# Performance work log

Hardware: AMD Instinct MI355X
Metric: run time of the kernel (lower is better)

## Reference

```python
import jax, jax.numpy as jnp
import numpy as np
from jax import lax

# Four fixed 3x3 directional difference kernels, stacked as OIHW [4,1,3,3]
_KL = np.array([[0, 0, 0], [-1, 1, 0], [0, 0, 0]], dtype=np.float32)
_KR = np.array([[0, 0, 0], [0, 1, -1], [0, 0, 0]], dtype=np.float32)
_KU = np.array([[0, -1, 0], [0, 1, 0], [0, 0, 0]], dtype=np.float32)
_KD = np.array([[0, 0, 0], [0, 1, 0], [0, -1, 0]], dtype=np.float32)
DIR_KERNELS = jnp.asarray(np.stack([_KL, _KR, _KU, _KD])[:, None, :, :])  # [4,1,3,3]


def _avg_pool4(x):
    # x: [B,1,H,W] with H,W divisible by 4 -> [B,1,H/4,W/4]
    B, C, H, W = x.shape
    return x.reshape(B, C, H // 4, 4, W // 4, 4).mean(axis=(3, 5))


def _dir_diffs(x):
    # x: [B,1,h,w] -> [B,4,h,w], 3x3 conv with zero padding 1 (SAME)
    return lax.conv_general_dilated(
        x, DIR_KERNELS,
        window_strides=(1, 1), padding=((1, 1), (1, 1)),
        dimension_numbers=('NCHW', 'OIHW', 'NCHW'))


def setup_inputs() -> dict:
    key = jax.random.key(0)
    k1, k2 = jax.random.split(key)
    org = jax.random.uniform(k1, (32, 3, 512, 512), dtype=jnp.float32)
    enhance = jax.random.uniform(k2, (32, 3, 512, 512), dtype=jnp.float32)
    return {"org": org, "enhance": enhance}


def reference(org, enhance):
    org_pool = _avg_pool4(org.mean(axis=1, keepdims=True))          # [B,1,h,w]
    enh_pool = _avg_pool4(enhance.mean(axis=1, keepdims=True))      # [B,1,h,w]
    d = _dir_diffs(org_pool) - _dir_diffs(enh_pool)                  # [B,4,h,w]
    E = jnp.sum(d * d, axis=1, keepdims=True)                        # [B,1,h,w]
    return E
```

## Files before the change

kernel.cpp:

```cpp
#include <hip/hip_runtime.h>


typedef float f4 __attribute__((ext_vector_type(4)));

__global__ __launch_bounds__(256) void pool_diff_kernel(
    const f4* __restrict__ org, const f4* __restrict__ enh,
    float* __restrict__ p) {
  __shared__ float red[128];
  int t = threadIdx.x;
  int s = blockIdx.x;
  int b = s >> 7;
  int py = s & 127;
  int sb = b * 196608 + py * 512;

  int j0 = sb + t;
  f4 A0 = __builtin_nontemporal_load(&org[j0]);
  f4 B0 = __builtin_nontemporal_load(&enh[j0]);
  f4 A1 = __builtin_nontemporal_load(&org[j0 + 65536]);
  f4 B1 = __builtin_nontemporal_load(&enh[j0 + 65536]);
  f4 A2 = __builtin_nontemporal_load(&org[j0 + 131072]);
  f4 B2 = __builtin_nontemporal_load(&enh[j0 + 131072]);
  f4 acc = (A0 - B0) + (A1 - B1) + (A2 - B2);

  int j1 = j0 + 256;
  f4 C0 = __builtin_nontemporal_load(&org[j1]);
  f4 D0 = __builtin_nontemporal_load(&enh[j1]);
  f4 C1 = __builtin_nontemporal_load(&org[j1 + 65536]);
  f4 D1 = __builtin_nontemporal_load(&enh[j1 + 65536]);
  f4 C2 = __builtin_nontemporal_load(&org[j1 + 131072]);
  f4 D2 = __builtin_nontemporal_load(&enh[j1 + 131072]);
  acc += (C0 - D0) + (C1 - D1) + (C2 - D2);

  float mine = acc.x + acc.y + acc.z + acc.w;
  if (t >= 128) red[t - 128] = mine;
  __syncthreads();
  if (t < 128) {
    p[b * 16384 + py * 128 + t] = (mine + red[t]) * (1.0f / 48.0f);
  }
}

__global__ __launch_bounds__(256) void espa_stencil_kernel(
    const float* __restrict__ p, float* __restrict__ out) {
  int idx = blockIdx.x * 256 + threadIdx.x;
  int x = idx & 127;
  int y = (idx >> 7) & 127;
  float c = p[idx];
  float l = (x > 0)   ? p[idx - 1]   : 0.f;
  float r = (x < 127) ? p[idx + 1]   : 0.f;
  float u = (y > 0)   ? p[idx - 128] : 0.f;
  float d = (y < 127) ? p[idx + 128] : 0.f;
  float dl = c - l, dr = c - r, du = c - u, dd = c - d;
  out[idx] = dl * dl + dr * dr + du * du + dd * dd;
}

extern "C" void kernel_launch(void* const* d_in, const int* in_sizes, int n_in,
                              void* d_out, int out_size, void* d_ws, size_t ws_size,
                              hipStream_t stream) {
  const f4* org = (const f4*)d_in[0];
  const f4* enh = (const f4*)d_in[1];
  float* p   = (float*)d_ws;
  float* out = (float*)d_out;

  pool_diff_kernel<<<4096, 256, 0, stream>>>(org, enh, p);
  const int N = 32 * 128 * 128;
  espa_stencil_kernel<<<N / 256, 256, 0, stream>>>(p, out);
}
```

Measured before the change: 197.4 us.

## Pool per channel with 16 loads in flight, sum channels in stencil

The pooling kernel now gives each block one channel of one image and four pooled rows. Each thread issues 16 independent vector loads instead of 12, which raises memory-level parallelism. The three per-channel pooled maps go to workspace, and the stencil kernel sums and scales them at each neighbor access. This trades a larger intermediate and about 15 scattered reads per output in the stencil for deeper load concurrency in the bandwidth-bound pass.

```diff
diff --git a/kernel.cpp b/kernel.cpp
--- a/kernel.cpp
+++ b/kernel.cpp
@@ -3,52 +3,77 @@
 
 typedef float f4 __attribute__((ext_vector_type(4)));
 
-__global__ __launch_bounds__(256) void pool_diff_kernel(
+__global__ __launch_bounds__(256) void pool_channel_kernel(
     const f4* __restrict__ org, const f4* __restrict__ enh,
-    float* __restrict__ p) {
-  __shared__ float red[128];
+    float* __restrict__ pc) {
+  __shared__ float red[4][128];
   int t = threadIdx.x;
   int s = blockIdx.x;
-  int b = s >> 7;
-  int py = s & 127;
-  int sb = b * 196608 + py * 512;
+  int g  = s & 31;
+  int bc = s >> 5;
+  int base = bc * 65536 + g * 2048;
 
-  int j0 = sb + t;
-  f4 A0 = __builtin_nontemporal_load(&org[j0]);
-  f4 B0 = __builtin_nontemporal_load(&enh[j0]);
-  f4 A1 = __builtin_nontemporal_load(&org[j0 + 65536]);
-  f4 B1 = __builtin_nontemporal_load(&enh[j0 + 65536]);
-  f4 A2 = __builtin_nontemporal_load(&org[j0 + 131072]);
-  f4 B2 = __builtin_nontemporal_load(&enh[j0 + 131072]);
-  f4 acc = (A0 - B0) + (A1 - B1) + (A2 - B2);
+  int h  = t >> 7;
+  int px = t & 127;
 
-  int j1 = j0 + 256;
-  f4 C0 = __builtin_nontemporal_load(&org[j1]);
-  f4 D0 = __builtin_nontemporal_load(&enh[j1]);
-  f4 C1 = __builtin_nontemporal_load(&org[j1 + 65536]);
-  f4 D1 = __builtin_nontemporal_load(&enh[j1 + 65536]);
-  f4 C2 = __builtin_nontemporal_load(&org[j1 + 131072]);
-  f4 D2 = __builtin_nontemporal_load(&enh[j1 + 131072]);
-  acc += (C0 - D0) + (C1 - D1) + (C2 - D2);
+  int j = base + t;
+  f4 o0 = __builtin_nontemporal_load(&org[j +    0]);
+  f4 o1 = __builtin_nontemporal_load(&org[j +  256]);
+  f4 o2 = __builtin_nontemporal_load(&org[j +  512]);
+  f4 o3 = __builtin_nontemporal_load(&org[j +  768]);
+  f4 o4 = __builtin_nontemporal_load(&org[j + 1024]);
+  f4 o5 = __builtin_nontemporal_load(&org[j + 1280]);
+  f4 o6 = __builtin_nontemporal_load(&org[j + 1536]);
+  f4 o7 = __builtin_nontemporal_load(&org[j + 1792]);
+  f4 e0 = __builtin_nontemporal_load(&enh[j +    0]);
+  f4 e1 = __builtin_nontemporal_load(&enh[j +  256]);
+  f4 e2 = __builtin_nontemporal_load(&enh[j +  512]);
+  f4 e3 = __builtin_nontemporal_load(&enh[j +  768]);
+  f4 e4 = __builtin_nontemporal_load(&enh[j + 1024]);
+  f4 e5 = __builtin_nontemporal_load(&enh[j + 1280]);
+  f4 e6 = __builtin_nontemporal_load(&enh[j + 1536]);
+  f4 e7 = __builtin_nontemporal_load(&enh[j + 1792]);
 
-  float mine = acc.x + acc.y + acc.z + acc.w;
-  if (t >= 128) red[t - 128] = mine;
+  f4 d0 = (o0 - e0) + (o1 - e1);
+  f4 d1 = (o2 - e2) + (o3 - e3);
+  f4 d2 = (o4 - e4) + (o5 - e5);
+  f4 d3 = (o6 - e6) + (o7 - e7);
+  float a0 = d0.x + d0.y + d0.z + d0.w;
+  float a1 = d1.x + d1.y + d1.z + d1.w;
+  float a2 = d2.x + d2.y + d2.z + d2.w;
+  float a3 = d3.x + d3.y + d3.z + d3.w;
+
+  if (h == 1) {
+    red[0][px] = a0; red[1][px] = a1; red[2][px] = a2; red[3][px] = a3;
+  }
   __syncthreads();
-  if (t < 128) {
-    p[b * 16384 + py * 128 + t] = (mine + red[t]) * (1.0f / 48.0f);
+  if (h == 0) {
+    int ob = bc * 16384 + g * 4 * 128 + px;
+    pc[ob +   0] = a0 + red[0][px];
+    pc[ob + 128] = a1 + red[1][px];
+    pc[ob + 256] = a2 + red[2][px];
+    pc[ob + 384] = a3 + red[3][px];
   }
 }
 
-__global__ __launch_bounds__(256) void espa_stencil_kernel(
-    const float* __restrict__ p, float* __restrict__ out) {
+__global__ __launch_bounds__(256) void combine_stencil_kernel(
+    const float* __restrict__ pc, float* __restrict__ out) {
   int idx = blockIdx.x * 256 + threadIdx.x;
   int x = idx & 127;
   int y = (idx >> 7) & 127;
-  float c = p[idx];
-  float l = (x > 0)   ? p[idx - 1]   : 0.f;
-  float r = (x < 127) ? p[idx + 1]   : 0.f;
-  float u = (y > 0)   ? p[idx - 128] : 0.f;
-  float d = (y < 127) ? p[idx + 128] : 0.f;
+  int b = idx >> 14;
+  const float* m0 = pc + (b * 3 + 0) * 16384;
+  const float* m1 = pc + (b * 3 + 1) * 16384;
+  const float* m2 = pc + (b * 3 + 2) * 16384;
+  int o = y * 128 + x;
+  auto P = [&](int oo) {
+    return (m0[oo] + m1[oo] + m2[oo]) * (1.0f / 48.0f);
+  };
+  float c = P(o);
+  float l = (x > 0)   ? P(o - 1)   : 0.f;
+  float r = (x < 127) ? P(o + 1)   : 0.f;
+  float u = (y > 0)   ? P(o - 128) : 0.f;
+  float d = (y < 127) ? P(o + 128) : 0.f;
   float dl = c - l, dr = c - r, du = c - u, dd = c - d;
   out[idx] = dl * dl + dr * dr + du * du + dd * dd;
 }
@@ -58,10 +83,10 @@
                               hipStream_t stream) {
   const f4* org = (const f4*)d_in[0];
   const f4* enh = (const f4*)d_in[1];
-  float* p   = (float*)d_ws;
+  float* pc  = (float*)d_ws;
   float* out = (float*)d_out;
 
-  pool_diff_kernel<<<4096, 256, 0, stream>>>(org, enh, p);
+  pool_channel_kernel<<<32 * 3 * 32, 256, 0, stream>>>(org, enh, pc);
   const int N = 32 * 128 * 128;
-  espa_stencil_kernel<<<N / 256, 256, 0, stream>>>(p, out);
+  combine_stencil_kernel<<<N / 256, 256, 0, stream>>>(pc, out);
 }
```

After: 198.1 us. About the same (+0.4%).
